# Kernel optimization log

Hardware: AMD Instinct MI355X
Metric: run time of the kernel (lower is better)

## Reference

```python
import jax, jax.numpy as jnp
import numpy as np

D_MODEL = 512
D_STATE = 128
D_CONV = 4
EXPAND = 2
HEADDIM = 64
D_INNER = EXPAND * D_MODEL            # 1024
NHEADS = D_INNER // HEADDIM           # 16
CONV_DIM = D_INNER + 2 * D_STATE      # 1280
D_IN_PROJ = 2 * D_INNER + 2 * D_STATE + NHEADS  # 2320
EPS = 1e-5


def _mamba2(u, in_w, conv_w, conv_b, A_log, dt_bias, Dp, norm_w, out_w):
    # u: [b, l, d_model]  -- Mamba2 forward (ngroups=1), SSD in exact quadratic form
    b, l, _ = u.shape
    zxbcdt = u @ in_w.T                                   # [b,l,2320]
    z = zxbcdt[..., :D_INNER]
    xBC = zxbcdt[..., D_INNER:D_INNER + CONV_DIM]
    dt = zxbcdt[..., D_INNER + CONV_DIM:]                 # [b,l,nheads]
    # causal depthwise conv1d (kernel 4) + silu
    xp = jnp.pad(xBC, ((0, 0), (D_CONV - 1, 0), (0, 0)))
    conv = sum(xp[:, k:k + l, :] * conv_w[:, k] for k in range(D_CONV))
    xBC = jax.nn.silu(conv + conv_b)
    x = xBC[..., :D_INNER].reshape(b, l, NHEADS, HEADDIM)
    Bm = xBC[..., D_INNER:D_INNER + D_STATE]              # [b,l,d_state]
    Cm = xBC[..., D_INNER + D_STATE:]                     # [b,l,d_state]
    dt = jax.nn.softplus(dt + dt_bias)                    # [b,l,nheads]
    dtA = dt * (-jnp.exp(A_log))                          # [b,l,nheads], negative
    # SSD quadratic (semiseparable) form: L[t,s] = exp(sum_{r=s+1..t} dtA_r), causal
    cs = jnp.cumsum(dtA, axis=1)                          # [b,l,nh]
    seg = cs[:, :, None, :] - cs[:, None, :, :]           # [b,t,s,nh]
    mask = jnp.tril(jnp.ones((l, l), bool))
    L = jnp.exp(jnp.where(mask[None, :, :, None], seg, -jnp.inf))
    G = jnp.einsum('btd,bsd->bts', Cm, Bm)                # C_t . B_s
    dtx = dt[..., None] * x                               # [b,l,nh,hd]
    y = jnp.einsum('btsn,bsnp->btnp', G[..., None] * L, dtx)
    y = (y + x * Dp[:, None]).reshape(b, l, D_INNER)      # D skip
    # gated RMSNorm (norm_before_gate=False): rmsnorm(y * silu(z)) * weight
    y = y * jax.nn.silu(z)
    y = y * jax.lax.rsqrt(jnp.mean(jnp.square(y), -1, keepdims=True) + EPS) * norm_w
    return y @ out_w.T


def _forward(x, h_in_w, h_conv_w, h_conv_b, h_A_log, h_dt_bias, h_D, h_norm_w, h_out_w,
             v_in_w, v_conv_w, v_conv_b, v_A_log, v_dt_bias, v_D, v_norm_w, v_out_w,
             fc_w, fc_b):
    B, H, W, C = x.shape
    hp = (h_in_w, h_conv_w, h_conv_b, h_A_log, h_dt_bias, h_D, h_norm_w, h_out_w)
    vp = (v_in_w, v_conv_w, v_conv_b, v_A_log, v_dt_bias, v_D, v_norm_w, v_out_w)
    # horizontal: scan along W for each (B*H) row
    xh = x.reshape(-1, W, C)
    h1 = _mamba2(xh, *hp)
    # NOTE: original code flips dim 0 (batch), reproduced faithfully
    h2 = jnp.flip(_mamba2(jnp.flip(xh, 0), *hp), 0)
    h = jnp.concatenate([h1, h2], -1).reshape(B, H, W, -1)
    # vertical: scan along H for each (B*W) column
    xv = jnp.transpose(x, (0, 2, 1, 3)).reshape(-1, H, C)
    v1 = _mamba2(xv, *vp)
    v2 = jnp.flip(_mamba2(jnp.flip(xv, 0), *vp), 0)
    v = jnp.transpose(jnp.concatenate([v1, v2], -1).reshape(B, W, H, -1), (0, 2, 1, 3))
    out = jnp.concatenate([v, h], -1) @ fc_w.T + fc_b     # [B,H,W,C]
    return out


def setup_inputs() -> dict:
    key = jax.random.key(0)
    ks = jax.random.split(key, 8)
    B, H, W, C = 2, 64, 64, D_MODEL
    x = jax.random.normal(ks[0], (B, H, W, C), jnp.float32)

    def mk(k):
        kk = jax.random.split(k, 5)
        return {
            'in_w': 0.02 * jax.random.normal(kk[0], (D_IN_PROJ, D_MODEL), jnp.float32),
            'conv_w': 0.1 * jax.random.normal(kk[1], (CONV_DIM, D_CONV), jnp.float32),
            'conv_b': jnp.zeros((CONV_DIM,), jnp.float32),
            'A_log': jnp.log(jax.random.uniform(kk[2], (NHEADS,), jnp.float32, 1.0, 16.0)),
            'dt_bias': jnp.log(jnp.expm1(jax.random.uniform(kk[3], (NHEADS,), jnp.float32, 1e-3, 0.1))),
            'D': jnp.ones((NHEADS,), jnp.float32),
            'norm_w': jnp.ones((D_INNER,), jnp.float32),
            'out_w': 0.02 * jax.random.normal(kk[4], (D_MODEL, D_INNER), jnp.float32),
        }

    hp, vp = mk(ks[1]), mk(ks[2])
    inp = {'x': x}
    inp.update({f'h_{n}': v for n, v in hp.items()})
    inp.update({f'v_{n}': v for n, v in vp.items()})
    inp['fc_w'] = 0.02 * jax.random.normal(ks[3], (D_MODEL, 4 * D_MODEL), jnp.float32)
    inp['fc_b'] = jnp.zeros((D_MODEL,), jnp.float32)
    return inp


def reference(x, h_in_w, h_conv_w, h_conv_b, h_A_log, h_dt_bias, h_D, h_norm_w, h_out_w,
              v_in_w, v_conv_w, v_conv_b, v_A_log, v_dt_bias, v_D, v_norm_w, v_out_w,
              fc_w, fc_b):
    return _forward(x, h_in_w, h_conv_w, h_conv_b, h_A_log, h_dt_bias, h_D, h_norm_w, h_out_w,
                    v_in_w, v_conv_w, v_conv_b, v_A_log, v_dt_bias, v_D, v_norm_w, v_out_w,
                    fc_w, fc_b)
```

## Files before the change

### kernel.cpp

```cpp
#include <hip/hip_runtime.h>

#define NROWS 8192
#define NZX   2304
#define BCS   136
#define XMS   72

#define PB0 4096
#define PB1 (PB0 + 2048)
#define PB2 (PB1 + 2304)
#define PB3 (PB2 + 256)
#define PB4 (PB3 + 512)

typedef __attribute__((ext_vector_type(8))) short bf16x8;
typedef __attribute__((ext_vector_type(4))) float f32x4;

__device__ __forceinline__ float bf2f(unsigned short u) {
    union { unsigned int i; float f; } v; v.i = ((unsigned int)u) << 16; return v.f;
}
__device__ __forceinline__ unsigned short f2bf(float f) {
    union { float f; unsigned int i; } v; v.f = f;
    return (unsigned short)((v.i + 0x8000u) >> 16);
}

__device__ __forceinline__ void async_lds16(const unsigned short* g, unsigned short* l) {
    __builtin_amdgcn_global_load_lds(
        (const __attribute__((address_space(1))) unsigned int*)g,
        (__attribute__((address_space(3))) unsigned int*)l, 16, 0, 0);
}

__global__ __launch_bounds__(256) void prep_kernel(
    const float* __restrict__ x, const float* __restrict__ fcw,
    const float* __restrict__ iw0, const float* __restrict__ iw1,
    const float* __restrict__ ow0, const float* __restrict__ ow1,
    const float* __restrict__ db0, const float* __restrict__ db1,
    const float* __restrict__ al0, const float* __restrict__ al1,
    unsigned short* __restrict__ xbf, unsigned short* __restrict__ wf,
    unsigned short* __restrict__ wbA, unsigned short* __restrict__ wbOT0,
    unsigned short* __restrict__ wbOT1, float* __restrict__ dtbb,
    float* __restrict__ csbb)
{
    __shared__ char sm[37888] __attribute__((aligned(16)));
    const int blk = blockIdx.x, tid = threadIdx.x;
    if (blk < PB0) {
        int i = blk * 256 + tid;
        float4 v = *(const float4*)(x + (size_t)i * 4);
        ushort4 o;
        o.x = f2bf(v.x); o.y = f2bf(v.y); o.z = f2bf(v.z); o.w = f2bf(v.w);
        *(ushort4*)(xbf + (size_t)i * 4) = o;
    } else if (blk < PB1) {
        int idx = (blk - PB0) * 256 + tid;
        int o = idx >> 10, c = idx & 1023;
        int half = c >> 9, cc = c & 511;
        float v = fcw[(size_t)o * 2048 + half * 1024 + cc] +
                  fcw[(size_t)o * 2048 + half * 1024 + 512 + cc];
        wf[idx] = f2bf(v);
    } else if (blk < PB2) {
        int local = blk - PB1;
        int dir = local / 1152;
        int i = (local % 1152) * 256 + tid;
        const float* s = dir ? iw1 : iw0;
        float4 v = *(const float4*)(s + (size_t)i * 4);
        ushort4 o;
        o.x = f2bf(v.x); o.y = f2bf(v.y); o.z = f2bf(v.z); o.w = f2bf(v.w);
        *(ushort4*)(wbA + (size_t)dir * (2304 * 512) + (size_t)i * 4) = o;
    } else if (blk < PB3) {
        float (*T)[65] = (float(*)[65])sm;
        int local = blk - PB2;
        int z = local >> 7, rem = local & 127;
        const float* s = z ? ow1 : ow0;
        unsigned short* d = z ? wbOT1 : wbOT0;
        const int bo = (rem >> 4) * 64, bc = (rem & 15) * 64;
#pragma unroll
        for (int i = 0; i < 16; ++i) {
            int slot = tid + i * 256;
            int r = slot >> 6, c = slot & 63;
            T[r][c] = s[(size_t)(bo + r) * 1024 + bc + c];
        }
        __syncthreads();
#pragma unroll
        for (int i = 0; i < 16; ++i) {
            int slot = tid + i * 256;
            int cr = slot >> 6, oc = slot & 63;
            d[(size_t)(bc + cr) * 512 + bo + oc] = f2bf(T[oc][cr]);
        }
    } else {
        float (*wsm)[512] = (float(*)[512])sm;
        float (*xs)[68]   = (float(*)[68])(sm + 16384);
        float (*dta)[64]  = (float(*)[64])(sm + 16384 + 17408);
        float (*dtt)[64]  = (float(*)[64])(sm + 16384 + 17408 + 2048);
        int local = blk - PB3;
        const int dir = local >> 8, bxl = local & 255;
        const float* in_w = dir ? iw1 : iw0;
        const float* dt_bias = dir ? db1 : db0;
        const float* A_log = dir ? al1 : al0;
        float* dtb = dtbb + (size_t)dir * 131072;
        float* csb = csbb + (size_t)dir * 131072;
        const int seq = bxl >> 1, hq = bxl & 1;
#pragma unroll
        for (int i = 0; i < 4; ++i) {
            int slot = tid + i * 256;
            int h = slot >> 7, c = (slot & 127) * 4;
            *(float4*)&wsm[h][c] = *(const float4*)(in_w + (size_t)(2304 + hq * 8 + h) * 512 + c);
        }
        const int t = tid & 63, hg = tid >> 6;
        float acc[2] = {0.f, 0.f};
        for (int c0 = 0; c0 < 512; c0 += 64) {
            __syncthreads();
#pragma unroll
            for (int i = 0; i < 4; ++i) {
                int slot = tid + i * 256;
                int r = slot >> 4, cc = (slot & 15) * 4;
                size_t row = (dir == 0) ? (size_t)seq * 64 + r
                                        : (size_t)(seq >> 6) * 4096 + (size_t)r * 64 + (seq & 63);
                *(float4*)&xs[r][cc] = *(const float4*)(x + row * 512 + c0 + cc);
            }
            __syncthreads();
#pragma unroll
            for (int cc = 0; cc < 64; cc += 4) {
                float4 u4 = *(const float4*)&xs[t][cc];
                const float* w0 = &wsm[hg * 2][c0 + cc];
                const float* w1 = &wsm[hg * 2 + 1][c0 + cc];
                acc[0] += u4.x * w0[0] + u4.y * w0[1] + u4.z * w0[2] + u4.w * w0[3];
                acc[1] += u4.x * w1[0] + u4.y * w1[1] + u4.z * w1[2] + u4.w * w1[3];
            }
        }
#pragma unroll
        for (int hh = 0; hh < 2; ++hh) {
            int hl = hg * 2 + hh;
            int h = hq * 8 + hl;
            float v = acc[hh] + dt_bias[h];
            float dtv = (v > 20.f) ? v : log1pf(__expf(v));
            dtt[hl][t] = dtv;
            dta[hl][t] = dtv * -__expf(A_log[h]);
        }
        __syncthreads();
        if (tid < 8) {
            float run = 0.f;
            int ob = (seq * 16 + hq * 8 + tid) * 64;
            for (int tt = 0; tt < 64; ++tt) {
                run += dta[tid][tt];
                dtb[ob + tt] = dtt[tid][tt];
                csb[ob + tt] = run;
            }
        }
    }
}

struct GemmEpi { unsigned short* C; int ldc; int colsub; int conv; };

template<int QA, bool LOADB>
__device__ __forceinline__ void mma_half(
    const unsigned short* Ab, const unsigned short* Bb,
    const int (&aoff)[4], const int (&boff)[2], const int (&kcx)[2],
    bf16x8 (&bv)[2][2][2], f32x4 (&acc)[8][4])
{
    bf16x8 av[4][2];
#pragma unroll
    for (int f = 0; f < 4; ++f)
#pragma unroll
        for (int kh = 0; kh < 2; ++kh)
            av[f][kh] = *(const bf16x8*)(Ab + QA * 8192 + aoff[f] + kcx[kh]);
    if (LOADB) {
#pragma unroll
        for (int h = 0; h < 2; ++h)
#pragma unroll
            for (int g = 0; g < 2; ++g)
#pragma unroll
                for (int kh = 0; kh < 2; ++kh)
                    bv[h][g][kh] = *(const bf16x8*)(Bb + h * 8192 + boff[g] + kcx[kh]);
    }
    __builtin_amdgcn_s_setprio(1);
#pragma unroll
    for (int f = 0; f < 4; ++f)
#pragma unroll
        for (int h = 0; h < 2; ++h)
#pragma unroll
            for (int g = 0; g < 2; ++g)
#pragma unroll
                for (int kh = 0; kh < 2; ++kh)
                    acc[QA * 4 + f][h * 2 + g] = __builtin_amdgcn_mfma_f32_16x16x32_bf16(
                        av[f][kh], bv[h][g][kh], acc[QA * 4 + f][h * 2 + g], 0, 0, 0);
    __builtin_amdgcn_s_setprio(0);
}

__global__ __launch_bounds__(512) void gemm_big(
    const unsigned short* __restrict__ xbf, const unsigned short* __restrict__ wbA,
    unsigned short* __restrict__ zx, const unsigned short* __restrict__ wf,
    const unsigned short* __restrict__ wbOT0, const unsigned short* __restrict__ wbOT1,
    unsigned short* __restrict__ wcomb, const float* __restrict__ cw0,
    const float* __restrict__ cw1, const float* __restrict__ cb0,
    const float* __restrict__ cb1, unsigned short* __restrict__ xbc)
{
    __shared__ unsigned short SMEM[65536] __attribute__((aligned(16)));
    unsigned short* AS = SMEM;
    unsigned short* BS = SMEM + 32768;
    const int bx = blockIdx.x, z = blockIdx.z;
    const unsigned short *A, *B;
    int lda, perm, mB, nB;
    GemmEpi epi;
    if (bx < 288) {
        int xcd = bx & 7, l = bx >> 3;
        int cid = xcd * 36 + l;
        int mt = cid / 9, nt = cid - mt * 9;
        mB = mt * 256; nB = nt * 256;
        A = xbf; lda = 512; perm = z;
        B = wbA + (size_t)z * (2304 * 512);
        if (nB >= 1024) { epi.C = xbc + (size_t)z * NROWS * 1280; epi.ldc = 1280; epi.colsub = 1024; epi.conv = 1; }
        else            { epi.C = zx + (size_t)z * NROWS * NZX;  epi.ldc = NZX;  epi.colsub = 0;    epi.conv = 0; }
    } else {
        int t2 = bx - 288;
        mB = (t2 >> 2) * 256; nB = (t2 & 3) * 256;
        A = z ? wf : wf + 512; lda = 1024; perm = 0;
        B = z ? wbOT1 : wbOT0;
        epi.C = z ? wcomb : wcomb + 1024; epi.ldc = 2048; epi.colsub = 0; epi.conv = 0;
    }
    const int tid = threadIdx.x, wave = tid >> 6, lane = tid & 63;
    const int wr = wave >> 2, wc = wave & 3;
    const int lr = lane & 15, lq = lane >> 4;
    const unsigned short* gA[2][2];
    const unsigned short* gB[2][2];
    int ldsSlot[2];
#pragma unroll
    for (int i = 0; i < 2; ++i) {
        int s = tid + i * 512;
        int r = s >> 3, p = s & 7, q = p ^ (r & 7);
        ldsSlot[i] = s * 8;
#pragma unroll
        for (int h = 0; h < 2; ++h) {
            int ar = mB + h * 128 + r;
            if (perm) ar = (ar & ~4095) | ((ar & 63) << 6) | ((ar >> 6) & 63);
            gA[i][h] = A + (size_t)ar * lda + q * 8;
            gB[i][h] = B + (size_t)(nB + h * 128 + r) * 512 + q * 8;
        }
    }
    int aoff[4], boff[2], kcx[2];
#pragma unroll
    for (int f = 0; f < 4; ++f) aoff[f] = (wr * 64 + f * 16 + lr) * 64;
#pragma unroll
    for (int g = 0; g < 2; ++g) boff[g] = (wc * 32 + g * 16 + lr) * 64;
#pragma unroll
    for (int kh = 0; kh < 2; ++kh) kcx[kh] = ((kh * 4 + lq) ^ (lr & 7)) * 8;
    f32x4 acc[8][4];
#pragma unroll
    for (int m = 0; m < 8; ++m)
#pragma unroll
        for (int n = 0; n < 4; ++n) acc[m][n] = (f32x4){0.f, 0.f, 0.f, 0.f};

#define STAGE_A(H, K0, CB) { _Pragma("unroll") \
    for (int i = 0; i < 2; ++i) async_lds16(gA[i][H] + (K0), AS + (CB) * 16384 + (H) * 8192 + ldsSlot[i]); }
#define STAGE_B(H, K0, CB) { _Pragma("unroll") \
    for (int i = 0; i < 2; ++i) async_lds16(gB[i][H] + (K0), BS + (CB) * 16384 + (H) * 8192 + ldsSlot[i]); }

    STAGE_A(0, 0, 0); STAGE_B(0, 0, 0); STAGE_B(1, 0, 0); STAGE_A(1, 0, 0);
#pragma unroll 1
    for (int t = 0; t < 7; ++t) {
        const int cb = t & 1, nb2 = cb ^ 1, k1 = (t + 1) * 64;
        const unsigned short* Ab = AS + cb * 16384;
        const unsigned short* Bb = BS + cb * 16384;
        bf16x8 bv[2][2][2];
        asm volatile("s_waitcnt vmcnt(2)" ::: "memory");
        asm volatile("s_barrier" ::: "memory");
        STAGE_A(0, k1, nb2); STAGE_B(0, k1, nb2);
        mma_half<0, true>(Ab, Bb, aoff, boff, kcx, bv, acc);
        asm volatile("s_waitcnt vmcnt(4)" ::: "memory");
        asm volatile("s_barrier" ::: "memory");
        STAGE_B(1, k1, nb2); STAGE_A(1, k1, nb2);
        mma_half<1, false>(Ab, Bb, aoff, boff, kcx, bv, acc);
    }
    {
        const unsigned short* Ab = AS + 16384;
        const unsigned short* Bb = BS + 16384;
        bf16x8 bv[2][2][2];
        asm volatile("s_waitcnt vmcnt(2)" ::: "memory");
        asm volatile("s_barrier" ::: "memory");
        mma_half<0, true>(Ab, Bb, aoff, boff, kcx, bv, acc);
        asm volatile("s_waitcnt vmcnt(0)" ::: "memory");
        asm volatile("s_barrier" ::: "memory");
        mma_half<1, false>(Ab, Bb, aoff, boff, kcx, bv, acc);
    }

    unsigned short* WR = BS + wave * 1024;
    const int rsl = (lane + 48) & 63;
    if (epi.conv) {
        float4 wv[4]; float bb[4];
#pragma unroll
        for (int c4 = 0; c4 < 4; ++c4) {
            int col = nB - 1024 + (c4 >> 1) * 128 + wc * 32 + (c4 & 1) * 16 + lr;
            const float* cwp = z ? cw1 : cw0;
            const float* cbp = z ? cb1 : cb0;
            wv[c4] = *(const float4*)(cwp + (size_t)col * 4);
            bb[c4] = cbp[col];
        }
#pragma unroll
        for (int h = 0; h < 2; ++h) {
            float pr1[4], pr2[4], pr3[4];
#pragma unroll
            for (int c4 = 0; c4 < 4; ++c4) { pr1[c4] = 0.f; pr2[c4] = 0.f; pr3[c4] = 0.f; }
#pragma unroll
            for (int f = 0; f < 4; ++f) {
#pragma unroll
                for (int c4 = 0; c4 < 4; ++c4) {
                    float vq[4];
#pragma unroll
                    for (int r = 0; r < 4; ++r) vq[r] = acc[h * 4 + f][c4][r];
                    float rc1 = __shfl(vq[1], rsl);
                    float rc2 = __shfl(vq[2], rsl);
                    float rc3 = __shfl(vq[3], rsl);
                    float u1 = lq ? rc3 : pr3[c4];
                    float u2 = lq ? rc2 : pr2[c4];
                    float u3 = lq ? rc1 : pr1[c4];
                    pr1[c4] = rc1; pr2[c4] = rc2; pr3[c4] = rc3;
                    float y4[4];
                    y4[0] = bb[c4] + wv[c4].w*vq[0] + wv[c4].z*u1    + wv[c4].y*u2    + wv[c4].x*u3;
                    y4[1] = bb[c4] + wv[c4].w*vq[1] + wv[c4].z*vq[0] + wv[c4].y*u1    + wv[c4].x*u2;
                    y4[2] = bb[c4] + wv[c4].w*vq[2] + wv[c4].z*vq[1] + wv[c4].y*vq[0] + wv[c4].x*u1;
                    y4[3] = bb[c4] + wv[c4].w*vq[3] + wv[c4].z*vq[2] + wv[c4].y*vq[1] + wv[c4].x*vq[0];
#pragma unroll
                    for (int r = 0; r < 4; ++r) {
                        float a = y4[r];
                        float s = a / (1.f + __expf(-a));
                        int r16 = lq * 4 + r;
                        int cn = c4 * 16 + lr;
                        int gp = ((cn >> 3) + (r16 >> 1)) & 7;
                        WR[r16 * 64 + gp * 8 + (cn & 7)] = f2bf(s);
                    }
                }
#pragma unroll
                for (int j = 0; j < 2; ++j) {
                    int r16 = j * 8 + (lane >> 3);
                    int gr = lane & 7;
                    int gp = (gr + (r16 >> 1)) & 7;
                    uint4 v = *(const uint4*)(WR + r16 * 64 + gp * 8);
                    int row = mB + h * 128 + wr * 64 + f * 16 + r16;
                    int col = nB - epi.colsub + (gr >> 2) * 128 + wc * 32 + ((gr >> 1) & 1) * 16 + (gr & 1) * 8;
                    *(uint4*)(epi.C + (size_t)row * epi.ldc + col) = v;
                }
            }
        }
    } else {
#pragma unroll
        for (int h = 0; h < 2; ++h)
#pragma unroll
            for (int f = 0; f < 4; ++f) {
#pragma unroll
                for (int c4 = 0; c4 < 4; ++c4)
#pragma unroll
                    for (int r = 0; r < 4; ++r) {
                        int r16 = lq * 4 + r;
                        int cn = c4 * 16 + lr;
                        int gp = ((cn >> 3) + (r16 >> 1)) & 7;
                        WR[r16 * 64 + gp * 8 + (cn & 7)] = f2bf(acc[h * 4 + f][c4][r]);
                    }
#pragma unroll
                for (int j = 0; j < 2; ++j) {
                    int r16 = j * 8 + (lane >> 3);
                    int gr = lane & 7;
                    int gp = (gr + (r16 >> 1)) & 7;
                    uint4 v = *(const uint4*)(WR + r16 * 64 + gp * 8);
                    int row = mB + h * 128 + wr * 64 + f * 16 + r16;
                    int col = nB + (gr >> 2) * 128 + wc * 32 + ((gr >> 1) & 1) * 16 + (gr & 1) * 8;
                    *(uint4*)(epi.C + (size_t)row * epi.ldc + col) = v;
                }
            }
    }
#undef STAGE_A
#undef STAGE_B
}

__global__ __launch_bounds__(256) void gemm_final2048(
    const unsigned short* __restrict__ YV, const unsigned short* __restrict__ YH,
    const unsigned short* __restrict__ W, const float* __restrict__ bias,
    float* __restrict__ C)
{
    __shared__ unsigned short As[128 * 64];
    __shared__ unsigned short Bs[64 * 64];
    const int tid = threadIdx.x, wave = tid >> 6, lane = tid & 63;
    const int did = blockIdx.y * 64 + blockIdx.x;
    const int mB = (did >> 3) * 128, nB = (did & 7) * 64;
    const int lr = lane & 15, lq = lane >> 4;
    int aq[4], agr[4], apr[4];
    unsigned short* lA[4];
    const unsigned short* BgP[2];
    unsigned short* lB[2];
#pragma unroll
    for (int i = 0; i < 4; ++i) {
        int s = tid + i * 256;
        int r = s >> 3, p = s & 7;
        aq[i] = (p ^ (r & 7)) * 8;
        int gr = mB + r;
        agr[i] = gr;
        apr[i] = (gr & ~4095) | ((gr & 63) << 6) | ((gr >> 6) & 63);
        lA[i] = As + s * 8;
    }
#pragma unroll
    for (int i = 0; i < 2; ++i) {
        int s = tid + i * 256;
        int r = s >> 3, p = s & 7;
        int q = p ^ (r & 7);
        BgP[i] = W + (size_t)(nB + r) * 2048 + q * 8;
        lB[i] = Bs + s * 8;
    }
    const int aswz = lr & 7;
    int arb[2], brb[4];
#pragma unroll
    for (int i = 0; i < 2; ++i) arb[i] = (wave * 32 + i * 16 + lr) * 64;
#pragma unroll
    for (int i = 0; i < 4; ++i) brb[i] = (i * 16 + lr) * 64;
    f32x4 zero4 = {0.f,0.f,0.f,0.f};
    f32x4 acc[2][4] = {{zero4,zero4,zero4,zero4},{zero4,zero4,zero4,zero4}};
    for (int k0 = 0; k0 < 2048; k0 += 64) {
#pragma unroll
        for (int i = 0; i < 4; ++i) {
            int kk = k0 + aq[i];
            const unsigned short* g = (kk < 1024)
                ? YV + (size_t)apr[i] * 1024 + kk
                : YH + (size_t)agr[i] * 1024 + (kk - 1024);
            async_lds16(g, lA[i]);
        }
#pragma unroll
        for (int i = 0; i < 2; ++i) async_lds16(BgP[i] + k0, lB[i]);
        __syncthreads();
#pragma unroll
        for (int kh = 0; kh < 2; ++kh) {
            const int ksw = ((kh * 4 + lq) ^ aswz) * 8;
            bf16x8 a[2], b[4];
#pragma unroll
            for (int i = 0; i < 2; ++i) a[i] = *(const bf16x8*)(As + arb[i] + ksw);
#pragma unroll
            for (int i = 0; i < 4; ++i) b[i] = *(const bf16x8*)(Bs + brb[i] + ksw);
#pragma unroll
            for (int mi = 0; mi < 2; ++mi)
#pragma unroll
                for (int ni = 0; ni < 4; ++ni)
                    acc[mi][ni] = __builtin_amdgcn_mfma_f32_16x16x32_bf16(
                        a[mi], b[ni], acc[mi][ni], 0, 0, 0);
        }
        __syncthreads();
    }
    const int rbase = lq * 4;
#pragma unroll
    for (int mi = 0; mi < 2; ++mi)
#pragma unroll
        for (int ni = 0; ni < 4; ++ni) {
            int col = nB + ni * 16 + lr;
            float bb = bias[col];
#pragma unroll
            for (int r = 0; r < 4; ++r) {
                int row = mB + wave * 32 + mi * 16 + rbase + r;
                C[(size_t)row * 512 + col] = acc[mi][ni][r] + bb;
            }
        }
}

__global__ __launch_bounds__(256) void gmat_kernel(
    const unsigned short* __restrict__ xbcb, float* __restrict__ Gbuf)
{
    __shared__ unsigned short Bs[64 * BCS];
    __shared__ unsigned short Cs[64 * BCS];
    const int dir = blockIdx.y, seq = blockIdx.x;
    const unsigned short* base = xbcb + (size_t)dir * NROWS * 1280
                                      + (size_t)seq * 64 * 1280;
    const int tid = threadIdx.x;
    const int lane = tid & 63, wave = tid >> 6;
#pragma unroll
    for (int i = 0; i < 4; ++i) {
        int e = (tid + i * 256) * 8;
        int r = e >> 7, c = e & 127;
        *(uint4*)(Bs + r * BCS + c) = *(const uint4*)(base + (size_t)r * 1280 + 1024 + c);
        *(uint4*)(Cs + r * BCS + c) = *(const uint4*)(base + (size_t)r * 1280 + 1152 + c);
    }
    __syncthreads();
    const int lr = lane & 15, lq = lane >> 4;
    f32x4 zero4 = {0.f,0.f,0.f,0.f};
    f32x4 acc[4] = {zero4, zero4, zero4, zero4};
#pragma unroll
    for (int kt = 0; kt < 4; ++kt) {
        bf16x8 a = *(const bf16x8*)(Cs + (wave * 16 + lr) * BCS + kt * 32 + lq * 8);
#pragma unroll
        for (int ni = 0; ni < 4; ++ni) {
            bf16x8 b = *(const bf16x8*)(Bs + (ni * 16 + lr) * BCS + kt * 32 + lq * 8);
            acc[ni] = __builtin_amdgcn_mfma_f32_16x16x32_bf16(a, b, acc[ni], 0, 0, 0);
        }
    }
    float* G = Gbuf + ((size_t)dir * 128 + seq) * 4096;
#pragma unroll
    for (int ni = 0; ni < 4; ++ni)
        *(f32x4*)(G + (ni * 16 + lr) * 64 + wave * 16 + lq * 4) = acc[ni];
}

__global__ __launch_bounds__(256) void scan_kernel(
    const unsigned short* __restrict__ xbcb, const float* __restrict__ Gbuf,
    const float* __restrict__ dtbb, const float* __restrict__ csbb,
    const float* __restrict__ Dv0, const float* __restrict__ Dv1,
    unsigned short* __restrict__ yh, unsigned short* __restrict__ yv)
{
    __shared__ unsigned short XsT[64 * XMS];
    __shared__ unsigned short Ms[64 * XMS];
    __shared__ float dts[64], css[64];
    const int dir = blockIdx.y;
    const unsigned short* xbc = xbcb + (size_t)dir * NROWS * 1280;
    const float* dtb = dtbb + (size_t)dir * 131072;
    const float* csb = csbb + (size_t)dir * 131072;
    const float* Dv = dir ? Dv1 : Dv0;
    unsigned short* y = dir ? yv : yh;
    const int tid = threadIdx.x;
    const int lane = tid & 63, wave = tid >> 6;
    const int seq = blockIdx.x >> 4, h = blockIdx.x & 15;
    if (tid < 64) {
        dts[tid] = dtb[(seq * 16 + h) * 64 + tid];
        css[tid] = csb[(seq * 16 + h) * 64 + tid];
    }
    const unsigned short* base = xbc + (size_t)seq * 64 * 1280;
#pragma unroll
    for (int i = 0; i < 2; ++i) {
        int e = (tid + i * 256) * 8;
        int t = e >> 6, p0 = e & 63;
        uint4 xval = *(const uint4*)(base + (size_t)t * 1280 + h * 64 + p0);
        const unsigned short* xs = (const unsigned short*)&xval;
#pragma unroll
        for (int j = 0; j < 8; ++j) {
            int jl = (j + lane) & 7;
            XsT[(p0 + jl) * XMS + t] = xs[jl];
        }
    }
    const int lr = lane & 15, lq = lane >> 4;
    const float* G = Gbuf + ((size_t)dir * 128 + seq) * 4096;
    f32x4 acc[4];
#pragma unroll
    for (int ni = 0; ni < 4; ++ni) {
        if (ni <= wave)
            acc[ni] = *(const f32x4*)(G + (ni * 16 + lr) * 64 + wave * 16 + lq * 4);
    }
    __syncthreads();
    float css_t[4];
#pragma unroll
    for (int r = 0; r < 4; ++r) css_t[r] = css[wave * 16 + lq * 4 + r];
    const int kmax = (wave < 2) ? 2 : 4;
#pragma unroll
    for (int ni = 0; ni < 4; ++ni) {
        int s = ni * 16 + lr;
        if (ni <= wave) {
            float cs_s = css[s], dt_s = dts[s];
#pragma unroll
            for (int r = 0; r < 4; ++r) {
                int t = wave * 16 + lq * 4 + r;
                float e = __expf(fminf(css_t[r] - cs_s, 0.f));
                float m = (s <= t) ? acc[ni][r] * e * dt_s : 0.f;
                Ms[t * XMS + s] = f2bf(m);
            }
        } else if (ni < kmax) {
#pragma unroll
            for (int r = 0; r < 4; ++r) {
                int t = wave * 16 + lq * 4 + r;
                Ms[t * XMS + s] = 0;
            }
        }
    }
    __syncthreads();
    f32x4 zero4 = {0.f,0.f,0.f,0.f};
    f32x4 yacc[4] = {zero4, zero4, zero4, zero4};
    const int ktn = (wave < 2) ? 1 : 2;
#pragma unroll
    for (int kt = 0; kt < 2; ++kt) {
        if (kt < ktn) {
            bf16x8 a = *(const bf16x8*)(Ms + (wave * 16 + lr) * XMS + kt * 32 + lq * 8);
#pragma unroll
            for (int ni = 0; ni < 4; ++ni) {
                bf16x8 b = *(const bf16x8*)(XsT + (ni * 16 + lr) * XMS + kt * 32 + lq * 8);
                yacc[ni] = __builtin_amdgcn_mfma_f32_16x16x32_bf16(a, b, yacc[ni], 0, 0, 0);
            }
        }
    }
    const float Dh = Dv[h];
#pragma unroll
    for (int ni = 0; ni < 4; ++ni) {
        int p = ni * 16 + lr;
#pragma unroll
        for (int r = 0; r < 4; ++r) {
            int t = wave * 16 + lq * 4 + r;
            float v = yacc[ni][r] + Dh * bf2f(XsT[p * XMS + t]);
            Ms[t * XMS + p] = f2bf(v);
        }
    }
    __syncthreads();
    unsigned short* yout = y + (size_t)seq * 64 * 1024 + h * 64;
#pragma unroll
    for (int i = 0; i < 2; ++i) {
        int slot = tid + i * 256;
        int t = slot >> 3, pc = (slot & 7) * 8;
        uint4 v = *(const uint4*)(Ms + t * XMS + pc);
        *(uint4*)(yout + (size_t)t * 1024 + pc) = v;
    }
}

__global__ __launch_bounds__(128) void gate_norm(
    const unsigned short* __restrict__ zxb, unsigned short* __restrict__ yh,
    unsigned short* __restrict__ yv, const float* __restrict__ nw0,
    const float* __restrict__ nw1)
{
    const int dir = blockIdx.y;
    const unsigned short* zx = zxb + (size_t)dir * NROWS * NZX;
    unsigned short* y = dir ? yv : yh;
    const float* nw = dir ? nw1 : nw0;
    const int row = blockIdx.x, tid = threadIdx.x;
    uint4 yv4 = *(const uint4*)(y + (size_t)row * 1024 + tid * 8);
    uint4 zv4 = *(const uint4*)(zx + (size_t)row * NZX + tid * 8);
    const unsigned short* ys = (const unsigned short*)&yv4;
    const unsigned short* zs = (const unsigned short*)&zv4;
    float g[8]; float ss = 0.f;
#pragma unroll
    for (int j = 0; j < 8; ++j) {
        float zv = bf2f(zs[j]);
        float gv = bf2f(ys[j]) * (zv / (1.f + __expf(-zv)));
        g[j] = gv; ss += gv * gv;
    }
#pragma unroll
    for (int off = 32; off > 0; off >>= 1) ss += __shfl_xor(ss, off, 64);
    __shared__ float red[2];
    if ((tid & 63) == 0) red[tid >> 6] = ss;
    __syncthreads();
    ss = red[0] + red[1];
    const float scale = rsqrtf(ss * (1.f / 1024.f) + 1e-5f);
    unsigned short out8[8] __attribute__((aligned(16)));
#pragma unroll
    for (int j = 0; j < 8; ++j) out8[j] = f2bf(g[j] * scale * nw[tid * 8 + j]);
    *(uint4*)(y + (size_t)row * 1024 + tid * 8) = *(const uint4*)out8;
}

extern "C" void kernel_launch(void* const* d_in, const int* in_sizes, int n_in,
                              void* d_out, int out_size, void* d_ws, size_t ws_size,
                              hipStream_t stream)
{
    (void)in_sizes; (void)n_in; (void)out_size; (void)ws_size;
    const float* x   = (const float*)d_in[0];
    const float* fcw = (const float*)d_in[17];
    const float* fcb = (const float*)d_in[18];
    const float* iw0 = (const float*)d_in[1];  const float* iw1 = (const float*)d_in[9];
    const float* cw0 = (const float*)d_in[2];  const float* cw1 = (const float*)d_in[10];
    const float* cb0 = (const float*)d_in[3];  const float* cb1 = (const float*)d_in[11];
    const float* al0 = (const float*)d_in[4];  const float* al1 = (const float*)d_in[12];
    const float* db0 = (const float*)d_in[5];  const float* db1 = (const float*)d_in[13];
    const float* Dv0 = (const float*)d_in[6];  const float* Dv1 = (const float*)d_in[14];
    const float* nw0 = (const float*)d_in[7];  const float* nw1 = (const float*)d_in[15];
    const float* ow0 = (const float*)d_in[8];  const float* ow1 = (const float*)d_in[16];

    char* ws = (char*)d_ws;
    size_t off = 0;
    auto alloc = [&](size_t bytes) {
        void* p = ws + off; off += (bytes + 255) & ~(size_t)255; return p;
    };
    unsigned short* xbf   = (unsigned short*)alloc((size_t)NROWS * 512 * 2);
    unsigned short* wbA   = (unsigned short*)alloc((size_t)2 * 2304 * 512 * 2);
    unsigned short* wbOT0 = (unsigned short*)alloc((size_t)1024 * 512 * 2);
    unsigned short* wbOT1 = (unsigned short*)alloc((size_t)1024 * 512 * 2);
    unsigned short* wf    = (unsigned short*)alloc((size_t)512 * 1024 * 2);
    unsigned short* wcomb = (unsigned short*)alloc((size_t)512 * 2048 * 2);
    unsigned short* zx    = (unsigned short*)alloc((size_t)2 * NROWS * NZX * 2);
    unsigned short* xbc   = (unsigned short*)alloc((size_t)2 * NROWS * 1280 * 2);
    float* Gbuf           = (float*)alloc((size_t)2 * 128 * 4096 * 4);
    float* dtb            = (float*)alloc((size_t)2 * 2048 * 64 * 4);
    float* csb            = (float*)alloc((size_t)2 * 2048 * 64 * 4);
    unsigned short* ybh   = (unsigned short*)alloc((size_t)NROWS * 1024 * 2);
    unsigned short* ybv   = (unsigned short*)alloc((size_t)NROWS * 1024 * 2);

    prep_kernel<<<PB4, 256, 0, stream>>>(x, fcw, iw0, iw1, ow0, ow1, db0, db1,
                                         al0, al1, xbf, wf, wbA, wbOT0, wbOT1,
                                         dtb, csb);
    gemm_big<<<dim3(296, 1, 2), 512, 0, stream>>>(xbf, wbA, zx, wf,
                                                  wbOT0, wbOT1, wcomb,
                                                  cw0, cw1, cb0, cb1, xbc);
    gmat_kernel<<<dim3(128, 2), 256, 0, stream>>>(xbc, Gbuf);
    scan_kernel<<<dim3(2048, 2), 256, 0, stream>>>(xbc, Gbuf, dtb, csb,
                                                   Dv0, Dv1, ybh, ybv);
    gate_norm<<<dim3(NROWS, 2), 128, 0, stream>>>(zx, ybh, ybv, nw0, nw1);
    gemm_final2048<<<dim3(64, 8), 256, 0, stream>>>(ybv, ybh, wcomb, fcb, (float*)d_out);
}
```

Baseline: 281.9 us.

## Fuse C·B Gram matrix computation into scan kernel, drop gmat kernel

```diff
diff --git a/kernel.cpp b/kernel.cpp
--- a/kernel.cpp
+++ b/kernel.cpp
@@ -452,50 +452,17 @@
         }
 }
 
-__global__ __launch_bounds__(256) void gmat_kernel(
-    const unsigned short* __restrict__ xbcb, float* __restrict__ Gbuf)
-{
-    __shared__ unsigned short Bs[64 * BCS];
-    __shared__ unsigned short Cs[64 * BCS];
-    const int dir = blockIdx.y, seq = blockIdx.x;
-    const unsigned short* base = xbcb + (size_t)dir * NROWS * 1280
-                                      + (size_t)seq * 64 * 1280;
-    const int tid = threadIdx.x;
-    const int lane = tid & 63, wave = tid >> 6;
-#pragma unroll
-    for (int i = 0; i < 4; ++i) {
-        int e = (tid + i * 256) * 8;
-        int r = e >> 7, c = e & 127;
-        *(uint4*)(Bs + r * BCS + c) = *(const uint4*)(base + (size_t)r * 1280 + 1024 + c);
-        *(uint4*)(Cs + r * BCS + c) = *(const uint4*)(base + (size_t)r * 1280 + 1152 + c);
-    }
-    __syncthreads();
-    const int lr = lane & 15, lq = lane >> 4;
-    f32x4 zero4 = {0.f,0.f,0.f,0.f};
-    f32x4 acc[4] = {zero4, zero4, zero4, zero4};
-#pragma unroll
-    for (int kt = 0; kt < 4; ++kt) {
-        bf16x8 a = *(const bf16x8*)(Cs + (wave * 16 + lr) * BCS + kt * 32 + lq * 8);
-#pragma unroll
-        for (int ni = 0; ni < 4; ++ni) {
-            bf16x8 b = *(const bf16x8*)(Bs + (ni * 16 + lr) * BCS + kt * 32 + lq * 8);
-            acc[ni] = __builtin_amdgcn_mfma_f32_16x16x32_bf16(a, b, acc[ni], 0, 0, 0);
-        }
-    }
-    float* G = Gbuf + ((size_t)dir * 128 + seq) * 4096;
-#pragma unroll
-    for (int ni = 0; ni < 4; ++ni)
-        *(f32x4*)(G + (ni * 16 + lr) * 64 + wave * 16 + lq * 4) = acc[ni];
-}
-
 __global__ __launch_bounds__(256) void scan_kernel(
-    const unsigned short* __restrict__ xbcb, const float* __restrict__ Gbuf,
+    const unsigned short* __restrict__ xbcb,
     const float* __restrict__ dtbb, const float* __restrict__ csbb,
     const float* __restrict__ Dv0, const float* __restrict__ Dv1,
     unsigned short* __restrict__ yh, unsigned short* __restrict__ yv)
 {
-    __shared__ unsigned short XsT[64 * XMS];
-    __shared__ unsigned short Ms[64 * XMS];
+    __shared__ char SM[2 * 64 * BCS * 2] __attribute__((aligned(16)));
+    unsigned short* Bs  = (unsigned short*)SM;
+    unsigned short* Cs  = (unsigned short*)(SM + 64 * BCS * 2);
+    unsigned short* XsT = (unsigned short*)SM;
+    unsigned short* Ms  = (unsigned short*)(SM + 64 * XMS * 2);
     __shared__ float dts[64], css[64];
     const int dir = blockIdx.y;
     const unsigned short* xbc = xbcb + (size_t)dir * NROWS * 1280;
@@ -512,6 +479,29 @@
     }
     const unsigned short* base = xbc + (size_t)seq * 64 * 1280;
 #pragma unroll
+    for (int i = 0; i < 4; ++i) {
+        int e = (tid + i * 256) * 8;
+        int r = e >> 7, c = e & 127;
+        *(uint4*)(Bs + r * BCS + c) = *(const uint4*)(base + (size_t)r * 1280 + 1024 + c);
+        *(uint4*)(Cs + r * BCS + c) = *(const uint4*)(base + (size_t)r * 1280 + 1152 + c);
+    }
+    __syncthreads();
+    const int lr = lane & 15, lq = lane >> 4;
+    f32x4 zero4 = {0.f,0.f,0.f,0.f};
+    f32x4 acc[4] = {zero4, zero4, zero4, zero4};
+#pragma unroll
+    for (int kt = 0; kt < 4; ++kt) {
+        bf16x8 a = *(const bf16x8*)(Cs + (wave * 16 + lr) * BCS + kt * 32 + lq * 8);
+#pragma unroll
+        for (int ni = 0; ni < 4; ++ni) {
+            if (ni <= wave) {
+                bf16x8 b = *(const bf16x8*)(Bs + (ni * 16 + lr) * BCS + kt * 32 + lq * 8);
+                acc[ni] = __builtin_amdgcn_mfma_f32_16x16x32_bf16(a, b, acc[ni], 0, 0, 0);
+            }
+        }
+    }
+    __syncthreads();
+#pragma unroll
     for (int i = 0; i < 2; ++i) {
         int e = (tid + i * 256) * 8;
         int t = e >> 6, p0 = e & 63;
@@ -523,15 +513,6 @@
             XsT[(p0 + jl) * XMS + t] = xs[jl];
         }
     }
-    const int lr = lane & 15, lq = lane >> 4;
-    const float* G = Gbuf + ((size_t)dir * 128 + seq) * 4096;
-    f32x4 acc[4];
-#pragma unroll
-    for (int ni = 0; ni < 4; ++ni) {
-        if (ni <= wave)
-            acc[ni] = *(const f32x4*)(G + (ni * 16 + lr) * 64 + wave * 16 + lq * 4);
-    }
-    __syncthreads();
     float css_t[4];
 #pragma unroll
     for (int r = 0; r < 4; ++r) css_t[r] = css[wave * 16 + lq * 4 + r];
@@ -557,7 +538,6 @@
         }
     }
     __syncthreads();
-    f32x4 zero4 = {0.f,0.f,0.f,0.f};
     f32x4 yacc[4] = {zero4, zero4, zero4, zero4};
     const int ktn = (wave < 2) ? 1 : 2;
 #pragma unroll
@@ -657,7 +637,6 @@
     unsigned short* wcomb = (unsigned short*)alloc((size_t)512 * 2048 * 2);
     unsigned short* zx    = (unsigned short*)alloc((size_t)2 * NROWS * NZX * 2);
     unsigned short* xbc   = (unsigned short*)alloc((size_t)2 * NROWS * 1280 * 2);
-    float* Gbuf           = (float*)alloc((size_t)2 * 128 * 4096 * 4);
     float* dtb            = (float*)alloc((size_t)2 * 2048 * 64 * 4);
     float* csb            = (float*)alloc((size_t)2 * 2048 * 64 * 4);
     unsigned short* ybh   = (unsigned short*)alloc((size_t)NROWS * 1024 * 2);
@@ -669,8 +648,7 @@
     gemm_big<<<dim3(296, 1, 2), 512, 0, stream>>>(xbf, wbA, zx, wf,
                                                   wbOT0, wbOT1, wcomb,
                                                   cw0, cw1, cb0, cb1, xbc);
-    gmat_kernel<<<dim3(128, 2), 256, 0, stream>>>(xbc, Gbuf);
-    scan_kernel<<<dim3(2048, 2), 256, 0, stream>>>(xbc, Gbuf, dtb, csb,
+    scan_kernel<<<dim3(2048, 2), 256, 0, stream>>>(xbc, dtb, csb,
                                                    Dv0, Dv1, ybh, ybv);
     gate_norm<<<dim3(NROWS, 2), 128, 0, stream>>>(zx, ybh, ybv, nw0, nw1);
     gemm_final2048<<<dim3(64, 8), 256, 0, stream>>>(ybv, ybh, wcomb, fcb, (float*)d_out);
```

New measurement: 293.4 us. 4.1% more time.
